# Performance work log

Hardware: AMD Instinct MI355X
Metric: run time of the kernel (lower is better)

Reference implementation:

```python
import jax, jax.numpy as jnp
import numpy as np

B, T, D, E, K = 4, 2048, 1024, 8, 2

def setup_inputs() -> dict:
    key = jax.random.key(0)
    ks = jax.random.split(key, 4)
    scale = 1.0 / np.sqrt(D)
    return {
        "input_feat": jax.random.normal(ks[0], (B, T, D), dtype=jnp.float32),
        "delta": jax.random.normal(ks[1], (B, T, D), dtype=jnp.float32),
        "gate_W": jax.random.normal(ks[2], (E, D), dtype=jnp.float32) * scale,
        "gate_b": jnp.zeros((E,), dtype=jnp.float32),
        "expert_W": jax.random.normal(ks[3], (E, D, D), dtype=jnp.float32) * scale,
        "expert_b": jnp.zeros((E, D), dtype=jnp.float32),
    }

def reference(input_feat, delta, gate_W, gate_b, expert_W, expert_b):
    # Gating: logits [B,T,E], top-k over experts, softmax over the k logits
    gate_logits = jnp.einsum("btd,ed->bte", input_feat, gate_W) + gate_b
    topk_vals, topk_idx = jax.lax.top_k(gate_logits, K)          # [B,T,K]
    topk_weights = jax.nn.softmax(topk_vals, axis=-1)            # [B,T,K]

    # Dense per-expert linear on delta: [B,T,D,E] (torch Linear: x @ W.T + b)
    expert_outputs = jnp.einsum("btd,efd->btfe", delta, expert_W) + expert_b.T

    # Gather top-k expert outputs and weighted-combine
    idx = jnp.broadcast_to(topk_idx[:, :, None, :], (B, T, D, K))
    topk_outputs = jnp.take_along_axis(expert_outputs, idx, axis=-1)  # [B,T,D,K]
    weighted_output = jnp.sum(topk_outputs * topk_weights[:, :, None, :], axis=-1)
    return weighted_output
```

## Files before the change

### kernel.cpp

```cpp
#include <hip/hip_runtime.h>
#include <hip/hip_fp16.h>
#include <stdint.h>

#define NTOK 8192
#define D 1024
#define E 8
#define BM 128
#define BN 64
#define BK 64

typedef __attribute__((ext_vector_type(8))) short short8;
typedef __attribute__((ext_vector_type(4))) float f32x4;

__device__ __forceinline__ ushort f2bf(float f) {
  uint32_t x = __float_as_uint(f);
  x += 0x7FFFu + ((x >> 16) & 1u);
  return (ushort)(x >> 16);
}

__device__ __forceinline__ ushort f2h(float f) {
  union { __half h; ushort u; } c;
  c.h = __float2half(f);
  return c.u;
}
__device__ __forceinline__ float h2f(ushort u) {
  union { __half h; ushort u; } c;
  c.u = u;
  return __half2float(c.h);
}

#define NW4 2097152
#define ND4 2097152
__global__ __launch_bounds__(256) void convert_kernel(
    const float* __restrict__ expert_W, const float* __restrict__ delta,
    ushort* __restrict__ Wb, ushort* __restrict__ Db, int* __restrict__ cnt) {
  int i = blockIdx.x * 256 + threadIdx.x;
  if (i < E) cnt[i] = 0;
  if (i < NW4) {
    float4 v = ((const float4*)expert_W)[i];
    ushort4 u; u.x = f2bf(v.x); u.y = f2bf(v.y); u.z = f2bf(v.z); u.w = f2bf(v.w);
    ((ushort4*)Wb)[i] = u;
  } else {
    int j = i - NW4;
    float4 v = ((const float4*)delta)[j];
    ushort4 u; u.x = f2bf(v.x); u.y = f2bf(v.y); u.z = f2bf(v.z); u.w = f2bf(v.w);
    ((ushort4*)Db)[j] = u;
  }
}

__global__ __launch_bounds__(256) void gatebin_kernel(
    const float* __restrict__ x, const float* __restrict__ gW,
    const float* __restrict__ gb, int* __restrict__ cnt,
    int* __restrict__ list, float* __restrict__ wlist) {
  int wave = threadIdx.x >> 6;
  int lane = threadIdx.x & 63;
  int tid = threadIdx.x;
  int t = blockIdx.x * 4 + wave;

  const float4* xr = (const float4*)(x + (size_t)t * D) + lane * 4;
  float acc[E];
#pragma unroll
  for (int e = 0; e < E; ++e) acc[e] = 0.f;
#pragma unroll
  for (int q = 0; q < 4; ++q) {
    float4 xv = xr[q];
#pragma unroll
    for (int e = 0; e < E; ++e) {
      float4 wv = ((const float4*)(gW + e * D))[lane * 4 + q];
      acc[e] += xv.x * wv.x + xv.y * wv.y + xv.z * wv.z + xv.w * wv.w;
    }
  }
#pragma unroll
  for (int e = 0; e < E; ++e) {
    float v = acc[e];
#pragma unroll
    for (int off = 32; off > 0; off >>= 1) v += __shfl_xor(v, off, 64);
    acc[e] = v;
  }

  __shared__ int sIdx[4];
  __shared__ float2 sW[4];
  __shared__ int hist[E];
  __shared__ int base[E];
  __shared__ int rofs[4][2];

  if (lane == 0) {
    float lg[E];
#pragma unroll
    for (int e = 0; e < E; ++e) lg[e] = acc[e] + gb[e];
    int i0 = 0; float v0 = lg[0];
#pragma unroll
    for (int e = 1; e < E; ++e) { if (lg[e] > v0) { v0 = lg[e]; i0 = e; } }
    int i1 = -1; float v1 = -1e30f;
#pragma unroll
    for (int e = 0; e < E; ++e) { if (e != i0 && lg[e] > v1) { v1 = lg[e]; i1 = e; } }
    float e1 = __expf(v1 - v0);
    float inv = 1.f / (1.f + e1);
    sIdx[wave] = i0 | (i1 << 16);
    sW[wave] = make_float2(inv, e1 * inv);
  }
  if (tid < E) hist[tid] = 0;
  __syncthreads();

  if (tid == 0) {
#pragma unroll
    for (int w4 = 0; w4 < 4; ++w4) {
      int p = sIdx[w4];
      rofs[w4][0] = hist[p & 0xFFFF]++;
      rofs[w4][1] = hist[p >> 16]++;
    }
  }
  __syncthreads();
  if (tid < E) base[tid] = hist[tid] ? atomicAdd(&cnt[tid], hist[tid]) : 0;
  __syncthreads();

  if (tid == 0) {
#pragma unroll
    for (int w4 = 0; w4 < 4; ++w4) {
      int p = sIdx[w4];
      int tk = blockIdx.x * 4 + w4;
      int e0 = p & 0xFFFF, e1 = p >> 16;
      int s0 = base[e0] + rofs[w4][0];
      list[e0 * NTOK + s0] = tk;
      wlist[e0 * NTOK + s0] = sW[w4].x;
      int s1 = base[e1] + rofs[w4][1];
      list[e1 * NTOK + s1] = tk | 0x80000000;
      wlist[e1 * NTOK + s1] = sW[w4].y;
    }
  }
}

__global__ __launch_bounds__(256) void moe_gemm_kernel(
    const ushort* __restrict__ Db, const ushort* __restrict__ Wb,
    const float* __restrict__ eb, const int* __restrict__ cnt,
    const int* __restrict__ list, const float* __restrict__ wlist,
    float* __restrict__ out) {
  int bx = blockIdx.x;
  int mt = bx >> 7;
  int rem = bx & 127;
  int e = rem >> 4;
  int nt = rem & 15;
  int M = cnt[e];
  int m0 = mt * BM;
  if (m0 >= M) return;
  int n0 = nt * BN;

  __shared__ ushort As[BM * BK];
  __shared__ ushort Bs[BN * BK];

  int tid = threadIdx.x;
  int wave = tid >> 6;
  int lane = tid & 63;
  int wm = wave >> 1;
  int wn = wave & 1;
  const int c = lane & 15;
  const int q = lane >> 4;

  const int* listE = list + e * NTOK;

  int rloc = lane >> 3;
  int gglob = (lane & 7) ^ rloc;
  const ushort* aptr[4];
  ushort* alds[4];
#pragma unroll
  for (int p = 0; p < 4; ++p) {
    int r = m0 + wave * 32 + p * 8 + rloc;
    int tok = listE[r < M ? r : m0] & 0x7FFFFFFF;
    aptr[p] = Db + (size_t)tok * D + gglob * 8;
    alds[p] = &As[(wave * 32 + p * 8) * BK];
  }
  const ushort* WbE = Wb + ((size_t)e << 20);
  const ushort* bptr[2];
  ushort* blds[2];
#pragma unroll
  for (int sub = 0; sub < 2; ++sub) {
    int row = n0 + wave * 16 + sub * 8 + rloc;
    bptr[sub] = WbE + (size_t)row * D + gglob * 8;
    blds[sub] = &Bs[(wave * 16 + sub * 8) * BK];
  }

  f32x4 acc[4][2];
#pragma unroll
  for (int i = 0; i < 4; ++i)
#pragma unroll
    for (int j = 0; j < 2; ++j)
      acc[i][j] = (f32x4){0.f, 0.f, 0.f, 0.f};

  for (int k0 = 0; k0 < D; k0 += BK) {
#pragma unroll
    for (int p = 0; p < 4; ++p)
      __builtin_amdgcn_global_load_lds(
          (const __attribute__((address_space(1))) void*)(aptr[p] + k0),
          (__attribute__((address_space(3))) void*)alds[p], 16, 0, 0);
#pragma unroll
    for (int sub = 0; sub < 2; ++sub)
      __builtin_amdgcn_global_load_lds(
          (const __attribute__((address_space(1))) void*)(bptr[sub] + k0),
          (__attribute__((address_space(3))) void*)blds[sub], 16, 0, 0);
    __syncthreads();

#pragma unroll
    for (int s = 0; s < 2; ++s) {
      int sw = (((s * 4 + q) ^ (c & 7)) * 8);
      short8 a[4], b[2];
#pragma unroll
      for (int i = 0; i < 4; ++i)
        a[i] = *(const short8*)&As[(wm * 64 + i * 16 + c) * BK + sw];
#pragma unroll
      for (int j = 0; j < 2; ++j)
        b[j] = *(const short8*)&Bs[(wn * 32 + j * 16 + c) * BK + sw];
#pragma unroll
      for (int i = 0; i < 4; ++i)
#pragma unroll
        for (int j = 0; j < 2; ++j)
          acc[i][j] = __builtin_amdgcn_mfma_f32_16x16x32_bf16(a[i], b[j], acc[i][j], 0, 0, 0);
    }
    __syncthreads();
  }

  float bias[2];
#pragma unroll
  for (int j = 0; j < 2; ++j)
    bias[j] = eb[e * D + n0 + wn * 32 + j * 16 + c];
  const float* wlE = wlist + e * NTOK;
  ushort* outh = (ushort*)out;
#pragma unroll
  for (int i = 0; i < 4; ++i) {
#pragma unroll
    for (int r = 0; r < 4; ++r) {
      int m = m0 + wm * 64 + i * 16 + q * 4 + r;
      if (m < M) {
        int en = listE[m];
        int tok = en & 0x7FFFFFFF;
        int rank = ((unsigned)en) >> 31;
        float w = wlE[m];
        size_t bi = ((size_t)tok * D + n0 + wn * 32 + c) * 2 + rank;
#pragma unroll
        for (int j = 0; j < 2; ++j)
          outh[bi + j * 32] = f2h((acc[i][j][r] + bias[j]) * w);
      }
    }
  }
}

#define NC4 2097152
__global__ __launch_bounds__(256) void combine_kernel(float* __restrict__ out) {
  int i = blockIdx.x * 256 + threadIdx.x;
  uint4 v = ((const uint4*)out)[i];
  float4 r;
  r.x = h2f((ushort)(v.x & 0xFFFF)) + h2f((ushort)(v.x >> 16));
  r.y = h2f((ushort)(v.y & 0xFFFF)) + h2f((ushort)(v.y >> 16));
  r.z = h2f((ushort)(v.z & 0xFFFF)) + h2f((ushort)(v.z >> 16));
  r.w = h2f((ushort)(v.w & 0xFFFF)) + h2f((ushort)(v.w >> 16));
  ((float4*)out)[i] = r;
}

extern "C" void kernel_launch(void* const* d_in, const int* in_sizes, int n_in,
                              void* d_out, int out_size, void* d_ws, size_t ws_size,
                              hipStream_t stream) {
  const float* input_feat = (const float*)d_in[0];
  const float* delta      = (const float*)d_in[1];
  const float* gate_W     = (const float*)d_in[2];
  const float* gate_b     = (const float*)d_in[3];
  const float* expert_W   = (const float*)d_in[4];
  const float* expert_b   = (const float*)d_in[5];
  float* out = (float*)d_out;

  char* ws = (char*)d_ws;
  ushort* Wb    = (ushort*)ws;
  ushort* Db    = (ushort*)(ws + 16777216);
  char*   meta  = ws + 2 * 16777216;
  int*    cnt   = (int*)meta;
  int*    list  = (int*)(meta + 256);
  float*  wlist = (float*)(meta + 256 + NTOK * E * 4);

  convert_kernel<<<(NW4 + ND4) / 256, 256, 0, stream>>>(expert_W, delta, Wb, Db, cnt);
  gatebin_kernel<<<NTOK / 4, 256, 0, stream>>>(input_feat, gate_W, gate_b, cnt, list, wlist);
  moe_gemm_kernel<<<(NTOK / BM) * 128, 256, 0, stream>>>(
      Db, Wb, expert_b, cnt, list, wlist, out);
  combine_kernel<<<NC4 / 256, 256, 0, stream>>>(out);
}
```

Measured before the change: 229.8 us.

## Double-buffer LDS tiles in MoE GEMM to overlap global loads with MFMA

Doubles the shared-memory A and B tile buffers in the expert GEMM. The first K tile is loaded before the loop, and each iteration issues direct-to-LDS loads for the next tile into the other buffer before running MFMAs on the current one. This aims to hide global-load latency behind matrix compute instead of stalling on a barrier before every tile. The cost is twice the LDS per block, which can lower occupancy, and it keeps one barrier per iteration.

```diff
diff --git a/kernel.cpp b/kernel.cpp
--- a/kernel.cpp
+++ b/kernel.cpp
@@ -8,6 +8,9 @@
 #define BM 128
 #define BN 64
 #define BK 64
+#define NKT (D / BK)
+#define ABUF (BM * BK)
+#define BBUF (BN * BK)
 
 typedef __attribute__((ext_vector_type(8))) short short8;
 typedef __attribute__((ext_vector_type(4))) float f32x4;
@@ -145,8 +148,8 @@
   if (m0 >= M) return;
   int n0 = nt * BN;
 
-  __shared__ ushort As[BM * BK];
-  __shared__ ushort Bs[BN * BK];
+  __shared__ ushort As[2 * ABUF];
+  __shared__ ushort Bs[2 * BBUF];
 
   int tid = threadIdx.x;
   int wave = tid >> 6;
@@ -186,29 +189,47 @@
     for (int j = 0; j < 2; ++j)
       acc[i][j] = (f32x4){0.f, 0.f, 0.f, 0.f};
 
-  for (int k0 = 0; k0 < D; k0 += BK) {
-#pragma unroll
-    for (int p = 0; p < 4; ++p)
-      __builtin_amdgcn_global_load_lds(
-          (const __attribute__((address_space(1))) void*)(aptr[p] + k0),
-          (__attribute__((address_space(3))) void*)alds[p], 16, 0, 0);
-#pragma unroll
-    for (int sub = 0; sub < 2; ++sub)
-      __builtin_amdgcn_global_load_lds(
-          (const __attribute__((address_space(1))) void*)(bptr[sub] + k0),
-          (__attribute__((address_space(3))) void*)blds[sub], 16, 0, 0);
-    __syncthreads();
-
+#pragma unroll
+  for (int p = 0; p < 4; ++p)
+    __builtin_amdgcn_global_load_lds(
+        (const __attribute__((address_space(1))) void*)(aptr[p]),
+        (__attribute__((address_space(3))) void*)(alds[p]), 16, 0, 0);
+#pragma unroll
+  for (int sub = 0; sub < 2; ++sub)
+    __builtin_amdgcn_global_load_lds(
+        (const __attribute__((address_space(1))) void*)(bptr[sub]),
+        (__attribute__((address_space(3))) void*)(blds[sub]), 16, 0, 0);
+  __syncthreads();
+
+  for (int kt = 0; kt < NKT; ++kt) {
+    int cur = kt & 1;
+    if (kt < NKT - 1) {
+      int nx = cur ^ 1;
+      int kk = (kt + 1) * BK;
+#pragma unroll
+      for (int p = 0; p < 4; ++p)
+        __builtin_amdgcn_global_load_lds(
+            (const __attribute__((address_space(1))) void*)(aptr[p] + kk),
+            (__attribute__((address_space(3))) void*)(alds[p] + nx * ABUF), 16, 0, 0);
+#pragma unroll
+      for (int sub = 0; sub < 2; ++sub)
+        __builtin_amdgcn_global_load_lds(
+            (const __attribute__((address_space(1))) void*)(bptr[sub] + kk),
+            (__attribute__((address_space(3))) void*)(blds[sub] + nx * BBUF), 16, 0, 0);
+    }
+
+    const ushort* Ab = As + cur * ABUF;
+    const ushort* Bb = Bs + cur * BBUF;
 #pragma unroll
     for (int s = 0; s < 2; ++s) {
       int sw = (((s * 4 + q) ^ (c & 7)) * 8);
       short8 a[4], b[2];
 #pragma unroll
       for (int i = 0; i < 4; ++i)
-        a[i] = *(const short8*)&As[(wm * 64 + i * 16 + c) * BK + sw];
+        a[i] = *(const short8*)&Ab[(wm * 64 + i * 16 + c) * BK + sw];
 #pragma unroll
       for (int j = 0; j < 2; ++j)
-        b[j] = *(const short8*)&Bs[(wn * 32 + j * 16 + c) * BK + sw];
+        b[j] = *(const short8*)&Bb[(wn * 32 + j * 16 + c) * BK + sw];
 #pragma unroll
       for (int i = 0; i < 4; ++i)
 #pragma unroll
```

New measurement: 240.2 us. 1.05x slower.
